# Kernel optimization log

Hardware: AMD Instinct MI355X
Metric: run time of the kernel (lower is better)

The kernel has to match this reference:

```python
import jax, jax.numpy as jnp
import numpy as np


def _hemisphere(radius=1.0, n=5):
    # replicates DiffuseShader.generate_hemisphere with sample=(5j,5j)
    u, v = np.mgrid[0:np.pi:n * 1j, 0:np.pi:n * 1j]
    x = (radius * np.cos(u) * np.sin(v)).flatten()
    y = (radius * np.sin(u) * np.sin(v)).flatten()
    z = (radius * np.cos(v)).flatten()
    return jnp.asarray(np.c_[x, y, z], dtype=jnp.float32)


def _diffuse_forward(V, COL, OPA, p, l, normals, hemi_vecs, indices, pointindex):
    P, S, N = p.shape[0], hemi_vecs.shape[0], V.shape[0]
    local = pointindex % P
    # --- project_hemisphere_projection: Rodrigues rotation local->global ---
    u = l[None, :] - p                                      # [P,3]
    u_hat = u / jnp.linalg.norm(u, axis=1, keepdims=True)
    v_loc = jnp.broadcast_to(jnp.array([0.0, -1.0, 0.0], p.dtype), u_hat.shape)
    c = -u_hat[:, 1:2]                                      # rowwise dot(v_loc, u_hat), [P,1]
    w = jnp.cross(v_loc, u_hat)                             # [P,3]
    z0 = jnp.zeros_like(w[:, 0])
    vmat = jnp.stack([jnp.stack([z0, -w[:, 2], w[:, 1]], -1),
                      jnp.stack([w[:, 2], z0, -w[:, 0]], -1),
                      jnp.stack([-w[:, 1], w[:, 0], z0], -1)], axis=1)  # [P,3,3] skew(w)
    R = jnp.eye(3, dtype=p.dtype)[None] + vmat + jnp.matmul(vmat, vmat) / (1.0 + c)[..., None]
    lh = jnp.einsum('pij,sj->psi', R, hemi_vecs) + l        # [P,S,3]
    o = jnp.broadcast_to(p[:, None, :], (P, S, 3))
    d = lh - o
    # --- get_intersection: ray/plane distances ---
    nrm = jnp.cross(V[:, 1] - V[:, 0], V[:, 2] - V[:, 0])
    nrm = nrm / jnp.linalg.norm(nrm, axis=1, keepdims=True)  # [N,3]
    kk = -jnp.sum(nrm * V[:, 3], axis=1)                     # [N]
    vo = o.reshape(P * S, 3) @ nrm.T                         # [P*S,N]
    vd = d.reshape(P * S, 3) @ nrm.T
    t = (-(kk[None, :] + vo) / vd).reshape(P, N, S)          # faithful to torch .view(P,N,S) on the [P*S,N] buffer
    surf = indices[pointindex, 0]
    mat = indices[pointindex, 1]
    empty = jnp.zeros((P, N, S), bool).at[local, surf, :].set(True)
    viable = (t > -1e-4) & (t < 1.0) & (~empty)
    # --- barycentric condition test ---
    r = o[:, None, :, :] + t[..., None] * d[:, None, :, :]   # [P,N,S,3]
    a0 = V[:, 0, 0][None, :, None]; a1 = V[:, 0, 1][None, :, None]; a2 = V[:, 0, 2][None, :, None]
    b0 = V[:, 1, 0][None, :, None]; b1 = V[:, 1, 1][None, :, None]; b2 = V[:, 1, 2][None, :, None]
    c0 = V[:, 2, 0][None, :, None]; c1 = V[:, 2, 1][None, :, None]; c2 = V[:, 2, 2][None, :, None]
    r0, r1, r2 = r[..., 0], r[..., 1], r[..., 2]
    A = a0 * r2 - a2 * r0
    B = a0 * b2 - a2 * b0
    C = a0 * r1 - a1 * r0
    D = a0 * b1 - a1 * b0
    E = a0 * c2 - a2 * c0
    F = B * (a1 * c0 - a0 * c1)
    gam = (D * (A * D - B * C)) / (D * (E * D + F))
    beta = (C + gam * (a1 * c0 - a0 * c1)) / D
    alpha = (r0 - (beta * b0 + gam * c0)) / a0
    mask = jnp.where(viable & (beta > 0.0) & (gam > 0.0) & (alpha > 0.0), 1.0, 0.0).astype(jnp.float32)
    col = COL[surf, mat]                                     # [P,3]
    opa = jnp.clip(OPA[surf, mat], 0.0, 1.0)                 # [P]
    reflected_ray = l[None, :] - p                           # [P,3]
    return mask, col, opa, reflected_ray


def setup_inputs() -> dict:
    P, N, M, G = 512, 1024, 8, 2048
    key = jax.random.key(0)
    ks = jax.random.split(key, 8)
    V = jax.random.normal(ks[0], (N, 4, 3), jnp.float32)
    indices = jax.random.randint(ks[1], (G, 2), 0, M)
    pointindex = jax.random.randint(ks[2], (P,), 0, G)
    COL = jax.random.uniform(ks[3], (N, M, 3), jnp.float32)
    OPA = jax.random.uniform(ks[4], (N, M), jnp.float32)
    p = jax.random.normal(ks[5], (P, 3), jnp.float32) * 5.0
    l = jax.random.normal(ks[6], (3,), jnp.float32) * 10.0 + 20.0
    normals = jax.random.normal(ks[7], (N, 3), jnp.float32)
    return {"V": V, "indices": indices, "pointindex": pointindex, "COL": COL,
            "OPA": OPA, "p": p, "l": l, "normals": normals, "it": 0,
            "hemi_vecs": _hemisphere(1.0, 5)}


def reference(V, indices, pointindex, COL, OPA, p, l, normals, it, hemi_vecs):
    return _diffuse_forward(V, COL, OPA, p, l, normals, hemi_vecs, indices, pointindex)
```

## Files before the change

### kernel.cpp

```cpp
#include <hip/hip_runtime.h>
#include <math.h>

#define NP   512
#define NT   1024
#define NS   25
#define NPS  (NP*NS)
#define MASKN (NP*NT*NS)

#define DSA_OFF  0
#define PD_OFF   51200
#define NX_OFF   53248
#define NY_OFF   54272
#define NZ_OFF   55296
#define KK_OFF   56320
#define W_OFF    57344
#define EMPTY_OFF ((size_t)67584 * 8)
#define F32_BYTE_OFF (EMPTY_OFF + 2048)
#define FD_OFF   0
#define FPD_OFF  51200
#define FNX_OFF  53248
#define FNY_OFF  54272
#define FNZ_OFF  55296
#define FKK_OFF  56320
#define FW_OFF   57344

#define CEPS 7.6293945e-06f

__device__ __forceinline__ double sgn(double x) {
    return (x > 0.0) ? 1.0 : ((x < 0.0) ? -1.0 : 0.0);
}

__global__ void prep_all(const float* __restrict__ p,
                         const float* __restrict__ l,
                         const float* __restrict__ hemi,
                         const float* __restrict__ V,
                         const int* __restrict__ indices,
                         const int* __restrict__ pointindex,
                         const float* __restrict__ COL,
                         const float* __restrict__ OPA,
                         double* __restrict__ ws,
                         unsigned* __restrict__ emptyMask,
                         float* __restrict__ out) {
    const int b = blockIdx.x, t = threadIdx.x;
    float* __restrict__ f32w = (float*)((char*)ws + F32_BYTE_OFF);
    if (b < 50) {
        int idx = b * 256 + t;
        int pi = idx / NS, si = idx % NS;
        double px = p[pi*3+0], py = p[pi*3+1], pz = p[pi*3+2];
        double lx = l[0], ly = l[1], lz = l[2];
        double ux = lx - px, uy = ly - py, uz = lz - pz;
        double nrm = sqrt(ux*ux + uy*uy + uz*uz);
        ux /= nrm; uy /= nrm; uz /= nrm;
        double c = -uy;
        double wx = -uz, wz = ux;
        double m01 = -wz, m10 = wz, m12 = -wx, m21 = wx;
        double q00 = m01*m10;
        double q02 = m01*m12;
        double q11 = m10*m01 + m12*m21;
        double q20 = m21*m10;
        double q22 = m21*m12;
        double ic = 1.0 + c;
        double r00 = 1.0 + q00/ic, r01 = m01,            r02 = q02/ic;
        double r10 = m10,          r11 = 1.0 + q11/ic,   r12 = m12;
        double r20 = q20/ic,       r21 = m21,            r22 = 1.0 + q22/ic;
        double hx = hemi[si*3+0], hy = hemi[si*3+1], hz = hemi[si*3+2];
        double dx = r00*hx + r01*hy + r02*hz + lx - px;
        double dy = r10*hx + r11*hy + r12*hz + ly - py;
        double dz = r20*hx + r21*hy + r22*hz + lz - pz;
        double* dsA = ws + DSA_OFF;
        dsA[idx*4+0] = dx;
        dsA[idx*4+1] = dy;
        dsA[idx*4+2] = dz;
        dsA[idx*4+3] = 0.0;
        *(float4*)(f32w + FD_OFF + idx*4) =
            make_float4((float)dx, (float)dy, (float)dz, 0.0f);
    } else if (b < 54) {
        int n = (b - 50) * 256 + t;
        const float* v = V + n*12;
        double a0=v[0], a1=v[1], a2=v[2];
        double b0=v[3], b1=v[4], b2=v[5];
        double c0=v[6], c1=v[7], c2=v[8];
        double v3x=v[9], v3y=v[10], v3z=v[11];
        double e1x=b0-a0, e1y=b1-a1, e1z=b2-a2;
        double e2x=c0-a0, e2y=c1-a1, e2z=c2-a2;
        double cx = e1y*e2z - e1z*e2y;
        double cy = e1z*e2x - e1x*e2z;
        double cz = e1x*e2y - e1y*e2x;
        double nn = sqrt(cx*cx + cy*cy + cz*cz);
        double nx = cx/nn, ny = cy/nn, nz = cz/nn;
        double kk = -(nx*v3x + ny*v3y + nz*v3z);
        double Bv = a0*b2 - a2*b0;
        double Dv = a0*b1 - a1*b0;
        double Ec = a0*c2 - a2*c0;
        double G2 = a1*c0 - a0*c1;
        double Fc = Bv*G2;
        double gd = Dv*(Ec*Dv + Fc);
        double gq = Dv*gd;
        double dq = Dv*c0;
        double aq = a0*gq;
        double WGr0 = a1*Bv - a2*Dv, WGr1 = -(a0*Bv), WGr2 = a0*Dv;
        double dg = Dv*G2;
        double WBr0 = -(a1*gd) + dg*WGr0;
        double WBr1 =  a0*gd  + dg*WGr1;
        double WBr2 =            dg*WGr2;
        double dd = Dv*dq;
        double WAr0 = gq - b0*WBr0 - dd*WGr0;
        double WAr1 =    - b0*WBr1 - dd*WGr1;
        double WAr2 =    - b0*WBr2 - dd*WGr2;
        double sg = sgn(Dv*gd), sb = sgn(gq), sa = sgn(aq);
        ws[NX_OFF + n] = nx;
        ws[NY_OFF + n] = ny;
        ws[NZ_OFF + n] = nz;
        ws[KK_OFF + n] = kk;
        double g0 = WGr0*sg, g1 = WGr1*sg, g2 = WGr2*sg;
        double bb0 = WBr0*sb, bb1 = WBr1*sb, bb2 = WBr2*sb;
        double aa0 = WAr0*sa, aa1 = WAr1*sa, aa2 = WAr2*sa;
        double* W = ws + W_OFF + n*10;
        W[0]=g0; W[1]=g1; W[2]=g2;
        W[3]=bb0; W[4]=bb1; W[5]=bb2;
        W[6]=aa0; W[7]=aa1; W[8]=aa2;
        W[9]=0.0;
        f32w[FNX_OFF+n]=(float)nx; f32w[FNY_OFF+n]=(float)ny;
        f32w[FNZ_OFF+n]=(float)nz; f32w[FKK_OFF+n]=(float)kk;
        double wsg = fabs(g0)+fabs(g1)+fabs(g2);
        double wsb = fabs(bb0)+fabs(bb1)+fabs(bb2);
        double wsa = fabs(aa0)+fabs(aa1)+fabs(aa2);
        double ig = wsg>0.0 ? 1.0/wsg : 0.0;
        double ib = wsb>0.0 ? 1.0/wsb : 0.0;
        double ia = wsa>0.0 ? 1.0/wsa : 0.0;
        float* fw = f32w + FW_OFF + n*12;
        fw[0]=(float)(g0*ig);  fw[1]=(float)(g1*ig);  fw[2]=(float)(g2*ig);
        fw[3]=(float)(bb0*ib); fw[4]=(float)(bb1*ib); fw[5]=(float)(bb2*ib);
        fw[6]=(float)(aa0*ia); fw[7]=(float)(aa1*ia); fw[8]=(float)(aa2*ia);
        fw[9]=0.0f; fw[10]=0.0f; fw[11]=0.0f;
    } else {
        emptyMask[t] = 0u;
        emptyMask[t + 256] = 0u;
        __syncthreads();
        for (int i = t; i < NP; i += 256) {
            int pidx = pointindex[i];
            int local = pidx & (NP - 1);
            int surf = indices[pidx*2 + 0];
            int mat  = indices[pidx*2 + 1];
            atomicOr(&emptyMask[local], 1u << surf);
            float* colOut = out + MASKN;
            float* opaOut = out + MASKN + 3*NP;
            float* refOut = out + MASKN + 4*NP;
            colOut[i*3+0] = COL[(surf*8+mat)*3+0];
            colOut[i*3+1] = COL[(surf*8+mat)*3+1];
            colOut[i*3+2] = COL[(surf*8+mat)*3+2];
            float o = OPA[surf*8+mat];
            opaOut[i] = fminf(fmaxf(o, 0.0f), 1.0f);
            refOut[i*3+0] = (float)((double)l[0] - (double)p[i*3+0]);
            refOut[i*3+1] = (float)((double)l[1] - (double)p[i*3+1]);
            refOut[i*3+2] = (float)((double)l[2] - (double)p[i*3+2]);
            double* pd = ws + PD_OFF;
            pd[i*4+0] = (double)p[i*3+0];
            pd[i*4+1] = (double)p[i*3+1];
            pd[i*4+2] = (double)p[i*3+2];
            pd[i*4+3] = 0.0;
            *(float4*)(f32w + FPD_OFF + i*4) =
                make_float4(p[i*3+0], p[i*3+1], p[i*3+2], 0.0f);
        }
    }
}

__device__ __forceinline__ float recheck64(const double* __restrict__ ws,
        unsigned ps, unsigned pp, unsigned i, unsigned nn, unsigned ss,
        unsigned em) {
    const double* s = ws + DSA_OFF + ps*4u;
    const double* o = ws + PD_OFF + pp*4u;
    double nx = ws[NX_OFF+i], ny = ws[NY_OFF+i], nz = ws[NZ_OFF+i];
    double kk = ws[KK_OFF+i];
    double vd = fma(s[2], nz, fma(s[1], ny, s[0]*nx));
    double tt = fma(o[2], nz, fma(o[1], ny, fma(o[0], nx, kk)));
    double e1 = fma(1e-4, vd, -tt);
    double e2 = vd + tt;
    const double* d = ws + DSA_OFF + (pp*25u + ss)*4u;
    double R0 = fma(-tt, d[0], vd*o[0]);
    double R1 = fma(-tt, d[1], vd*o[1]);
    double R2 = fma(-tt, d[2], vd*o[2]);
    const double* w = ws + W_OFF + nn*10u;
    double dG = fma(R2, w[2], fma(R1, w[1], R0*w[0]));
    double dB = fma(R2, w[5], fma(R1, w[4], R0*w[3]));
    double dA = fma(R2, w[8], fma(R1, w[7], R0*w[6]));
    int hv = __double2hiint(vd);
    int m = (__double2hiint(e1)^hv) | (__double2hiint(e2)^hv)
          | (__double2hiint(dG)^hv) | (__double2hiint(dB)^hv)
          | (__double2hiint(dA)^hv);
    bool ok = (m >= 0) && !((nn < 8u) && ((em >> nn) & 1u));
    return ok ? 1.0f : 0.0f;
}

__global__ __launch_bounds__(256, 4) void diffuse_main(
        const double* __restrict__ ws,
        const unsigned* __restrict__ emptyMask,
        float* __restrict__ out) {
    __shared__ float sW[42][12];
    __shared__ float sdx[25], sdy[25], sdz[25], sdm[25];

    const float* __restrict__ f32 = (const float*)((const char*)ws + F32_BYTE_OFF);
    const unsigned ps = blockIdx.x;
    const unsigned pp = ps / 25u;
    const unsigned q  = ps - pp*25u;
    const unsigned nn0 = (q << 10) / 25u;
    const unsigned tid = threadIdx.x;
    const unsigned n0 = tid * 4u;

    const float4 fnx = *(const float4*)(f32 + FNX_OFF + n0);
    const float4 fny = *(const float4*)(f32 + FNY_OFF + n0);
    const float4 fnz = *(const float4*)(f32 + FNZ_OFF + n0);
    const float4 fkk = *(const float4*)(f32 + FKK_OFF + n0);
    const float sx = f32[FD_OFF + ps*4u + 0];
    const float sy = f32[FD_OFF + ps*4u + 1];
    const float sz = f32[FD_OFF + ps*4u + 2];
    const float ox = f32[FPD_OFF + pp*4u + 0];
    const float oy = f32[FPD_OFF + pp*4u + 1];
    const float oz = f32[FPD_OFF + pp*4u + 2];
    const unsigned em = (q == 0u) ? emptyMask[pp] : 0u;
    const float S1u = fabsf(sx) + fabsf(sy) + fabsf(sz);
    const float O1u = fabsf(ox) + fabsf(oy) + fabsf(oz);
    const float Evd = CEPS * S1u;
    const float Eb0 = S1u + O1u;
    const float SOu = S1u * O1u;

    if (tid < 126u) {
        unsigned row = tid / 3u, quad = tid - row*3u;
        unsigned gn = nn0 + row; if (gn > 1023u) gn = 1023u;
        const float4 v = *(const float4*)(f32 + FW_OFF + gn*12u + quad*4u);
        *(float4*)(&sW[row][quad*4u]) = v;
    }
    if (tid < 25u) {
        const float4 dr = *(const float4*)(f32 + FD_OFF + (pp*25u + tid)*4u);
        sdx[tid] = dr.x; sdy[tid] = dr.y; sdz[tid] = dr.z;
        sdm[tid] = fmaxf(fabsf(dr.x), fmaxf(fabsf(dr.y), fabsf(dr.z)));
    }
    __syncthreads();

    const float nxk[4] = {fnx.x, fnx.y, fnx.z, fnx.w};
    const float nyk[4] = {fny.x, fny.y, fny.z, fny.w};
    const float nzk[4] = {fnz.x, fnz.y, fnz.z, fnz.w};
    const float kkk[4] = {fkk.x, fkk.y, fkk.z, fkk.w};

    unsigned rem = (q << 10) + n0;
    unsigned nn = rem / 25u;
    unsigned ss = rem - nn*25u;

    float res[4];
    #pragma unroll
    for (int k = 0; k < 4; ++k) {
        const float nx = nxk[k], ny = nyk[k], nz = nzk[k], kk = kkk[k];
        const float vd = fmaf(sz, nz, fmaf(sy, ny, sx*nx));
        const float tt = fmaf(oz, nz, fmaf(oy, ny, fmaf(ox, nx, kk)));
        const float e1 = fmaf(1e-4f, vd, -tt);
        const float e2 = vd + tt;

        const float dxv = sdx[ss], dyv = sdy[ss], dzv = sdz[ss], dmv = sdm[ss];
        const float R0 = fmaf(-tt, dxv, vd*ox);
        const float R1 = fmaf(-tt, dyv, vd*oy);
        const float R2 = fmaf(-tt, dzv, vd*oz);

        const float* w = sW[nn - nn0];
        const float dG = fmaf(R2, w[2], fmaf(R1, w[1], R0*w[0]));
        const float dB = fmaf(R2, w[5], fmaf(R1, w[4], R0*w[3]));
        const float dA = fmaf(R2, w[8], fmaf(R1, w[7], R0*w[6]));

        const int hv = __float_as_int(vd);
        int msk = (__float_as_int(e1)^hv) | (__float_as_int(e2)^hv)
                | (__float_as_int(dG)^hv) | (__float_as_int(dB)^hv)
                | (__float_as_int(dA)^hv);
        bool ok = (msk >= 0) && !((nn < 8u) && ((em >> nn) & 1u));

        const float akk = fabsf(kk);
        const float Ee  = CEPS * (Eb0 + akk);
        const float Mtt = O1u + akk;
        const float MR  = fmaf(Mtt, dmv, SOu);
        const float Edx = CEPS * MR;
        const float mind = fminf(fabsf(dG), fminf(fabsf(dB), fabsf(dA)));
        const bool flag = (fabsf(vd) < Evd) | (fabsf(e1) < Ee)
                        | (fabsf(e2) < Ee) | (mind < Edx);

        float r = ok ? 1.0f : 0.0f;
        if (__builtin_expect(flag, 0))
            r = recheck64(ws, ps, pp, n0 + (unsigned)k, nn, ss, em);
        res[k] = r;

        ss += 1u;
        const bool wrap = (ss == 25u);
        nn += wrap ? 1u : 0u;
        ss  = wrap ? 0u : ss;
    }
    *(float4*)(out + (ps << 10) + n0) = make_float4(res[0], res[1], res[2], res[3]);
}

extern "C" void kernel_launch(void* const* d_in, const int* in_sizes, int n_in,
                              void* d_out, int out_size, void* d_ws, size_t ws_size,
                              hipStream_t stream) {
    const float* V         = (const float*)d_in[0];
    const int*   indices   = (const int*)  d_in[1];
    const int*   pointindex= (const int*)  d_in[2];
    const float* COL       = (const float*)d_in[3];
    const float* OPA       = (const float*)d_in[4];
    const float* p         = (const float*)d_in[5];
    const float* l         = (const float*)d_in[6];
    const float* hemi      = (const float*)d_in[9];

    float* out = (float*)d_out;
    double* ws = (double*)d_ws;
    unsigned* emptyMask = (unsigned*)((char*)d_ws + EMPTY_OFF);

    prep_all<<<55, 256, 0, stream>>>(p, l, hemi, V, indices, pointindex,
                                     COL, OPA, ws, emptyMask, out);
    diffuse_main<<<NPS, 256, 0, stream>>>(ws, emptyMask, out);
}
```

Baseline: 33.65 us.

## Restructure main kernel to per-point blocks with per-triangle weights in registers and bitmask output

Each block now handles half of one point's 1024 triangles instead of one (point, sample) row. Each thread keeps two triangles' edge weights in registers and loops over all 25 samples, reusing those weights. Normals are staged in shared memory, and results are packed into 25-bit masks before a shared-memory transpose produces coalesced float2 stores. The fp64 recheck becomes a noinline function run per flagged bit, which cuts register pressure on the common path. The cost is more shared memory, a second barrier and more index arithmetic.

```diff
diff --git a/kernel.cpp b/kernel.cpp
--- a/kernel.cpp
+++ b/kernel.cpp
@@ -165,13 +165,12 @@
     }
 }
 
-__device__ __forceinline__ float recheck64(const double* __restrict__ ws,
-        unsigned ps, unsigned pp, unsigned i, unsigned nn, unsigned ss,
-        unsigned em) {
+__device__ __noinline__ unsigned recheck64(const double* __restrict__ ws,
+        unsigned ps, unsigned pp, unsigned n, unsigned nn, unsigned ss) {
     const double* s = ws + DSA_OFF + ps*4u;
     const double* o = ws + PD_OFF + pp*4u;
-    double nx = ws[NX_OFF+i], ny = ws[NY_OFF+i], nz = ws[NZ_OFF+i];
-    double kk = ws[KK_OFF+i];
+    double nx = ws[NX_OFF+n], ny = ws[NY_OFF+n], nz = ws[NZ_OFF+n];
+    double kk = ws[KK_OFF+n];
     double vd = fma(s[2], nz, fma(s[1], ny, s[0]*nx));
     double tt = fma(o[2], nz, fma(o[1], ny, fma(o[0], nx, kk)));
     double e1 = fma(1e-4, vd, -tt);
@@ -188,109 +187,138 @@
     int m = (__double2hiint(e1)^hv) | (__double2hiint(e2)^hv)
           | (__double2hiint(dG)^hv) | (__double2hiint(dB)^hv)
           | (__double2hiint(dA)^hv);
-    bool ok = (m >= 0) && !((nn < 8u) && ((em >> nn) & 1u));
-    return ok ? 1.0f : 0.0f;
+    return (m >= 0) ? 1u : 0u;
 }
 
 __global__ __launch_bounds__(256, 4) void diffuse_main(
         const double* __restrict__ ws,
         const unsigned* __restrict__ emptyMask,
         float* __restrict__ out) {
-    __shared__ float sW[42][12];
-    __shared__ float sdx[25], sdy[25], sdz[25], sdm[25];
+    __shared__ __align__(16) float snx[NT], sny[NT], snz[NT], skk[NT];
+    __shared__ float4 sdr[NS];
+    __shared__ unsigned sbits[512];
 
     const float* __restrict__ f32 = (const float*)((const char*)ws + F32_BYTE_OFF);
-    const unsigned ps = blockIdx.x;
-    const unsigned pp = ps / 25u;
-    const unsigned q  = ps - pp*25u;
-    const unsigned nn0 = (q << 10) / 25u;
+    const unsigned pp = blockIdx.x >> 1;
+    const unsigned half = blockIdx.x & 1u;
     const unsigned tid = threadIdx.x;
-    const unsigned n0 = tid * 4u;
-
-    const float4 fnx = *(const float4*)(f32 + FNX_OFF + n0);
-    const float4 fny = *(const float4*)(f32 + FNY_OFF + n0);
-    const float4 fnz = *(const float4*)(f32 + FNZ_OFF + n0);
-    const float4 fkk = *(const float4*)(f32 + FKK_OFF + n0);
-    const float sx = f32[FD_OFF + ps*4u + 0];
-    const float sy = f32[FD_OFF + ps*4u + 1];
-    const float sz = f32[FD_OFF + ps*4u + 2];
+    const unsigned nnA = half*512u + tid;
+    const unsigned nnB = nnA + 256u;
+
+    const float4 wA0 = *(const float4*)(f32 + FW_OFF + nnA*12u);
+    const float4 wA1 = *(const float4*)(f32 + FW_OFF + nnA*12u + 4u);
+    const float4 wA2 = *(const float4*)(f32 + FW_OFF + nnA*12u + 8u);
+    const float4 wB0 = *(const float4*)(f32 + FW_OFF + nnB*12u);
+    const float4 wB1 = *(const float4*)(f32 + FW_OFF + nnB*12u + 4u);
+    const float4 wB2 = *(const float4*)(f32 + FW_OFF + nnB*12u + 8u);
     const float ox = f32[FPD_OFF + pp*4u + 0];
     const float oy = f32[FPD_OFF + pp*4u + 1];
     const float oz = f32[FPD_OFF + pp*4u + 2];
-    const unsigned em = (q == 0u) ? emptyMask[pp] : 0u;
-    const float S1u = fabsf(sx) + fabsf(sy) + fabsf(sz);
+    const unsigned em = emptyMask[pp];
+
+    {
+        const unsigned i4 = tid * 4u;
+        *(float4*)&snx[i4] = *(const float4*)(f32 + FNX_OFF + i4);
+        *(float4*)&sny[i4] = *(const float4*)(f32 + FNY_OFF + i4);
+        *(float4*)&snz[i4] = *(const float4*)(f32 + FNZ_OFF + i4);
+        *(float4*)&skk[i4] = *(const float4*)(f32 + FKK_OFF + i4);
+    }
+    if (tid < 25u) {
+        float4 dr = *(const float4*)(f32 + FD_OFF + (pp*25u + tid)*4u);
+        dr.w = fmaxf(fabsf(dr.x), fmaxf(fabsf(dr.y), fabsf(dr.z)));
+        sdr[tid] = dr;
+    }
+    __syncthreads();
+
     const float O1u = fabsf(ox) + fabsf(oy) + fabsf(oz);
-    const float Evd = CEPS * S1u;
-    const float Eb0 = S1u + O1u;
-    const float SOu = S1u * O1u;
-
-    if (tid < 126u) {
-        unsigned row = tid / 3u, quad = tid - row*3u;
-        unsigned gn = nn0 + row; if (gn > 1023u) gn = 1023u;
-        const float4 v = *(const float4*)(f32 + FW_OFF + gn*12u + quad*4u);
-        *(float4*)(&sW[row][quad*4u]) = v;
-    }
-    if (tid < 25u) {
-        const float4 dr = *(const float4*)(f32 + FD_OFF + (pp*25u + tid)*4u);
-        sdx[tid] = dr.x; sdy[tid] = dr.y; sdz[tid] = dr.z;
-        sdm[tid] = fmaxf(fabsf(dr.x), fmaxf(fabsf(dr.y), fabsf(dr.z)));
+
+    #pragma unroll
+    for (int h = 0; h < 2; ++h) {
+        const unsigned nn = h ? nnB : nnA;
+        const float4 w0 = h ? wB0 : wA0;
+        const float4 w1 = h ? wB1 : wA1;
+        const float4 w2 = h ? wB2 : wA2;
+        const unsigned m0  = nn * 25u;
+        const unsigned n0  = m0 & 1023u;
+        const unsigned ps0 = m0 >> 10;
+        const unsigned idx1 = (m0 + 24u) >> 10;
+        const unsigned ssX = ((ps0 + 1u) << 10) - m0;
+        const float4 s0v = sdr[ps0];
+        const float4 s1v = sdr[idx1];
+        const float S10 = fabsf(s0v.x) + fabsf(s0v.y) + fabsf(s0v.z);
+        const float S11 = fabsf(s1v.x) + fabsf(s1v.y) + fabsf(s1v.z);
+
+        unsigned acc = 0u, flg = 0u;
+        #pragma unroll 5
+        for (unsigned ss = 0u; ss < 25u; ++ss) {
+            const bool cr = (ss >= ssX);
+            const float sx = cr ? s1v.x : s0v.x;
+            const float sy = cr ? s1v.y : s0v.y;
+            const float sz = cr ? s1v.z : s0v.z;
+            const float S1u = cr ? S11 : S10;
+            const unsigned n = n0 + ss - (cr ? 1024u : 0u);
+            const float nx = snx[n], ny = sny[n], nz = snz[n], kk = skk[n];
+
+            const float vd = fmaf(sz, nz, fmaf(sy, ny, sx*nx));
+            const float tt = fmaf(oz, nz, fmaf(oy, ny, fmaf(ox, nx, kk)));
+            const float e1 = fmaf(1e-4f, vd, -tt);
+            const float e2 = vd + tt;
+
+            const float4 d4 = sdr[ss];
+            const float R0 = fmaf(-tt, d4.x, vd*ox);
+            const float R1 = fmaf(-tt, d4.y, vd*oy);
+            const float R2 = fmaf(-tt, d4.z, vd*oz);
+
+            const float dG = fmaf(R2, w0.z, fmaf(R1, w0.y, R0*w0.x));
+            const float dB = fmaf(R2, w1.y, fmaf(R1, w1.x, R0*w0.w));
+            const float dA = fmaf(R2, w2.x, fmaf(R1, w1.w, R0*w1.z));
+
+            const int hv = __float_as_int(vd);
+            const int msk = (__float_as_int(e1)^hv) | (__float_as_int(e2)^hv)
+                          | (__float_as_int(dG)^hv) | (__float_as_int(dB)^hv)
+                          | (__float_as_int(dA)^hv);
+            acc |= ((unsigned)(msk >= 0)) << ss;
+
+            const float akk = fabsf(kk);
+            const float Ee  = CEPS * (S1u + O1u + akk);
+            const float Mtt = O1u + akk;
+            const float MR  = fmaf(Mtt, d4.w, S1u * O1u);
+            const float Edx = CEPS * MR;
+            const float mind = fminf(fabsf(dG), fminf(fabsf(dB), fabsf(dA)));
+            const bool flag = (fabsf(vd) < CEPS*S1u) | (fabsf(e1) < Ee)
+                            | (fabsf(e2) < Ee) | (mind < Edx);
+            flg |= ((unsigned)flag) << ss;
+        }
+        if (__builtin_expect(flg != 0u, 0)) {
+            unsigned f2 = flg;
+            while (f2) {
+                const unsigned ss = (unsigned)__ffs(f2) - 1u;
+                f2 &= f2 - 1u;
+                const bool cr = (ss >= ssX);
+                const unsigned n = n0 + ss - (cr ? 1024u : 0u);
+                const unsigned ps = pp*25u + ps0 + (cr ? 1u : 0u);
+                const unsigned bit = recheck64(ws, ps, pp, n, nn, ss);
+                acc = (acc & ~(1u << ss)) | (bit << ss);
+            }
+        }
+        if ((nn < 8u) && ((em >> nn) & 1u)) acc = 0u;
+        sbits[h*256u + tid] = acc;
     }
     __syncthreads();
 
-    const float nxk[4] = {fnx.x, fnx.y, fnx.z, fnx.w};
-    const float nyk[4] = {fny.x, fny.y, fny.z, fny.w};
-    const float nzk[4] = {fnz.x, fnz.y, fnz.z, fnz.w};
-    const float kkk[4] = {fkk.x, fkk.y, fkk.z, fkk.w};
-
-    unsigned rem = (q << 10) + n0;
-    unsigned nn = rem / 25u;
-    unsigned ss = rem - nn*25u;
-
-    float res[4];
-    #pragma unroll
-    for (int k = 0; k < 4; ++k) {
-        const float nx = nxk[k], ny = nyk[k], nz = nzk[k], kk = kkk[k];
-        const float vd = fmaf(sz, nz, fmaf(sy, ny, sx*nx));
-        const float tt = fmaf(oz, nz, fmaf(oy, ny, fmaf(ox, nx, kk)));
-        const float e1 = fmaf(1e-4f, vd, -tt);
-        const float e2 = vd + tt;
-
-        const float dxv = sdx[ss], dyv = sdy[ss], dzv = sdz[ss], dmv = sdm[ss];
-        const float R0 = fmaf(-tt, dxv, vd*ox);
-        const float R1 = fmaf(-tt, dyv, vd*oy);
-        const float R2 = fmaf(-tt, dzv, vd*oz);
-
-        const float* w = sW[nn - nn0];
-        const float dG = fmaf(R2, w[2], fmaf(R1, w[1], R0*w[0]));
-        const float dB = fmaf(R2, w[5], fmaf(R1, w[4], R0*w[3]));
-        const float dA = fmaf(R2, w[8], fmaf(R1, w[7], R0*w[6]));
-
-        const int hv = __float_as_int(vd);
-        int msk = (__float_as_int(e1)^hv) | (__float_as_int(e2)^hv)
-                | (__float_as_int(dG)^hv) | (__float_as_int(dB)^hv)
-                | (__float_as_int(dA)^hv);
-        bool ok = (msk >= 0) && !((nn < 8u) && ((em >> nn) & 1u));
-
-        const float akk = fabsf(kk);
-        const float Ee  = CEPS * (Eb0 + akk);
-        const float Mtt = O1u + akk;
-        const float MR  = fmaf(Mtt, dmv, SOu);
-        const float Edx = CEPS * MR;
-        const float mind = fminf(fabsf(dG), fminf(fabsf(dB), fabsf(dA)));
-        const bool flag = (fabsf(vd) < Evd) | (fabsf(e1) < Ee)
-                        | (fabsf(e2) < Ee) | (mind < Edx);
-
-        float r = ok ? 1.0f : 0.0f;
-        if (__builtin_expect(flag, 0))
-            r = recheck64(ws, ps, pp, n0 + (unsigned)k, nn, ss, em);
-        res[k] = r;
-
-        ss += 1u;
-        const bool wrap = (ss == 25u);
-        nn += wrap ? 1u : 0u;
-        ss  = wrap ? 0u : ss;
-    }
-    *(float4*)(out + (ps << 10) + n0) = make_float4(res[0], res[1], res[2], res[3]);
+    const unsigned obase = pp*25600u + half*12800u;
+    #pragma unroll 5
+    for (unsigned it = 0u; it < 25u; ++it) {
+        const unsigned j = (it*256u + tid) * 2u;
+        const unsigned nn1 = j / 25u;
+        const unsigned ss1 = j - nn1*25u;
+        const unsigned j2 = j + 1u;
+        const unsigned nn2 = j2 / 25u;
+        const unsigned ss2 = j2 - nn2*25u;
+        const float r0 = ((sbits[nn1] >> ss1) & 1u) ? 1.0f : 0.0f;
+        const float r1 = ((sbits[nn2] >> ss2) & 1u) ? 1.0f : 0.0f;
+        *(float2*)(out + obase + j) = make_float2(r0, r1);
+    }
 }
 
 extern "C" void kernel_launch(void* const* d_in, const int* in_sizes, int n_in,
@@ -311,5 +339,5 @@
 
     prep_all<<<55, 256, 0, stream>>>(p, l, hemi, V, indices, pointindex,
                                      COL, OPA, ws, emptyMask, out);
-    diffuse_main<<<NPS, 256, 0, stream>>>(ws, emptyMask, out);
-}
+    diffuse_main<<<NP*2, 256, 0, stream>>>(ws, emptyMask, out);
+}
```

Result: slower. 38.94 us (+15.7%).

## Load plane weights into registers, defer fp64 rechecks to a noinline loop

Applied to the files above, without the earlier changes.

The shared-memory staging of per-triangle edge weights is dropped. Each thread now loads the two weight rows it can touch (nnA and nnB) straight into registers, and the per-sample direction table becomes a float4 array in shared memory. The fp64 recheck is no longer called inline inside the unrolled loop: flags are packed into a bitmask and rechecked afterwards through a noinline function, with the minimum-occupancy hint removed from launch bounds. The goal is fewer LDS reads, a smaller shared footprint and lower register pressure on the common path. The cost is more global loads per thread and a function call on the rare path.

```diff
diff --git a/kernel.cpp b/kernel.cpp
--- a/kernel.cpp
+++ b/kernel.cpp
@@ -165,13 +165,12 @@
     }
 }
 
-__device__ __forceinline__ float recheck64(const double* __restrict__ ws,
-        unsigned ps, unsigned pp, unsigned i, unsigned nn, unsigned ss,
-        unsigned em) {
+__device__ __noinline__ unsigned recheck64(const double* __restrict__ ws,
+        unsigned ps, unsigned pp, unsigned n, unsigned nn, unsigned ss) {
     const double* s = ws + DSA_OFF + ps*4u;
     const double* o = ws + PD_OFF + pp*4u;
-    double nx = ws[NX_OFF+i], ny = ws[NY_OFF+i], nz = ws[NZ_OFF+i];
-    double kk = ws[KK_OFF+i];
+    double nx = ws[NX_OFF+n], ny = ws[NY_OFF+n], nz = ws[NZ_OFF+n];
+    double kk = ws[KK_OFF+n];
     double vd = fma(s[2], nz, fma(s[1], ny, s[0]*nx));
     double tt = fma(o[2], nz, fma(o[1], ny, fma(o[0], nx, kk)));
     double e1 = fma(1e-4, vd, -tt);
@@ -188,25 +187,33 @@
     int m = (__double2hiint(e1)^hv) | (__double2hiint(e2)^hv)
           | (__double2hiint(dG)^hv) | (__double2hiint(dB)^hv)
           | (__double2hiint(dA)^hv);
-    bool ok = (m >= 0) && !((nn < 8u) && ((em >> nn) & 1u));
-    return ok ? 1.0f : 0.0f;
-}
-
-__global__ __launch_bounds__(256, 4) void diffuse_main(
+    return (m >= 0) ? 1u : 0u;
+}
+
+__global__ __launch_bounds__(256) void diffuse_main(
         const double* __restrict__ ws,
         const unsigned* __restrict__ emptyMask,
         float* __restrict__ out) {
-    __shared__ float sW[42][12];
-    __shared__ float sdx[25], sdy[25], sdz[25], sdm[25];
+    __shared__ float4 sdr[NS];
 
     const float* __restrict__ f32 = (const float*)((const char*)ws + F32_BYTE_OFF);
     const unsigned ps = blockIdx.x;
     const unsigned pp = ps / 25u;
     const unsigned q  = ps - pp*25u;
-    const unsigned nn0 = (q << 10) / 25u;
     const unsigned tid = threadIdx.x;
     const unsigned n0 = tid * 4u;
 
+    const unsigned rem0 = (q << 10) + n0;
+    const unsigned nnA = rem0 / 25u;
+    const unsigned ssA = rem0 - nnA*25u;
+    const unsigned nnB = (nnA < 1023u) ? (nnA + 1u) : 1023u;
+
+    const float4 wA0 = *(const float4*)(f32 + FW_OFF + nnA*12u);
+    const float4 wA1 = *(const float4*)(f32 + FW_OFF + nnA*12u + 4u);
+    const float4 wA2 = *(const float4*)(f32 + FW_OFF + nnA*12u + 8u);
+    const float4 wB0 = *(const float4*)(f32 + FW_OFF + nnB*12u);
+    const float4 wB1 = *(const float4*)(f32 + FW_OFF + nnB*12u + 4u);
+    const float4 wB2 = *(const float4*)(f32 + FW_OFF + nnB*12u + 8u);
     const float4 fnx = *(const float4*)(f32 + FNX_OFF + n0);
     const float4 fny = *(const float4*)(f32 + FNY_OFF + n0);
     const float4 fnz = *(const float4*)(f32 + FNZ_OFF + n0);
@@ -218,77 +225,86 @@
     const float oy = f32[FPD_OFF + pp*4u + 1];
     const float oz = f32[FPD_OFF + pp*4u + 2];
     const unsigned em = (q == 0u) ? emptyMask[pp] : 0u;
+
+    if (tid < 25u) {
+        float4 dr = *(const float4*)(f32 + FD_OFF + (pp*25u + tid)*4u);
+        dr.w = fmaxf(fabsf(dr.x), fmaxf(fabsf(dr.y), fabsf(dr.z)));
+        sdr[tid] = dr;
+    }
+    __syncthreads();
+
     const float S1u = fabsf(sx) + fabsf(sy) + fabsf(sz);
     const float O1u = fabsf(ox) + fabsf(oy) + fabsf(oz);
+    const float SOu = S1u * O1u;
     const float Evd = CEPS * S1u;
-    const float Eb0 = S1u + O1u;
-    const float SOu = S1u * O1u;
-
-    if (tid < 126u) {
-        unsigned row = tid / 3u, quad = tid - row*3u;
-        unsigned gn = nn0 + row; if (gn > 1023u) gn = 1023u;
-        const float4 v = *(const float4*)(f32 + FW_OFF + gn*12u + quad*4u);
-        *(float4*)(&sW[row][quad*4u]) = v;
-    }
-    if (tid < 25u) {
-        const float4 dr = *(const float4*)(f32 + FD_OFF + (pp*25u + tid)*4u);
-        sdx[tid] = dr.x; sdy[tid] = dr.y; sdz[tid] = dr.z;
-        sdm[tid] = fmaxf(fabsf(dr.x), fmaxf(fabsf(dr.y), fabsf(dr.z)));
-    }
-    __syncthreads();
 
     const float nxk[4] = {fnx.x, fnx.y, fnx.z, fnx.w};
     const float nyk[4] = {fny.x, fny.y, fny.z, fny.w};
     const float nzk[4] = {fnz.x, fnz.y, fnz.z, fnz.w};
     const float kkk[4] = {fkk.x, fkk.y, fkk.z, fkk.w};
 
-    unsigned rem = (q << 10) + n0;
-    unsigned nn = rem / 25u;
-    unsigned ss = rem - nn*25u;
-
     float res[4];
+    unsigned flg = 0u;
     #pragma unroll
     for (int k = 0; k < 4; ++k) {
+        const bool useB = (ssA + (unsigned)k >= 25u);
+        const unsigned ss = ssA + (unsigned)k - (useB ? 25u : 0u);
+        const unsigned nn = useB ? nnB : nnA;
+        const float wg0 = useB ? wB0.x : wA0.x;
+        const float wg1 = useB ? wB0.y : wA0.y;
+        const float wg2 = useB ? wB0.z : wA0.z;
+        const float wb0 = useB ? wB0.w : wA0.w;
+        const float wb1 = useB ? wB1.x : wA1.x;
+        const float wb2 = useB ? wB1.y : wA1.y;
+        const float wa0 = useB ? wB1.z : wA1.z;
+        const float wa1 = useB ? wB1.w : wA1.w;
+        const float wa2 = useB ? wB2.x : wA2.x;
+
         const float nx = nxk[k], ny = nyk[k], nz = nzk[k], kk = kkk[k];
         const float vd = fmaf(sz, nz, fmaf(sy, ny, sx*nx));
         const float tt = fmaf(oz, nz, fmaf(oy, ny, fmaf(ox, nx, kk)));
         const float e1 = fmaf(1e-4f, vd, -tt);
         const float e2 = vd + tt;
 
-        const float dxv = sdx[ss], dyv = sdy[ss], dzv = sdz[ss], dmv = sdm[ss];
-        const float R0 = fmaf(-tt, dxv, vd*ox);
-        const float R1 = fmaf(-tt, dyv, vd*oy);
-        const float R2 = fmaf(-tt, dzv, vd*oz);
-
-        const float* w = sW[nn - nn0];
-        const float dG = fmaf(R2, w[2], fmaf(R1, w[1], R0*w[0]));
-        const float dB = fmaf(R2, w[5], fmaf(R1, w[4], R0*w[3]));
-        const float dA = fmaf(R2, w[8], fmaf(R1, w[7], R0*w[6]));
+        const float4 d4 = sdr[ss];
+        const float R0 = fmaf(-tt, d4.x, vd*ox);
+        const float R1 = fmaf(-tt, d4.y, vd*oy);
+        const float R2 = fmaf(-tt, d4.z, vd*oz);
+
+        const float dG = fmaf(R2, wg2, fmaf(R1, wg1, R0*wg0));
+        const float dB = fmaf(R2, wb2, fmaf(R1, wb1, R0*wb0));
+        const float dA = fmaf(R2, wa2, fmaf(R1, wa1, R0*wa0));
 
         const int hv = __float_as_int(vd);
-        int msk = (__float_as_int(e1)^hv) | (__float_as_int(e2)^hv)
-                | (__float_as_int(dG)^hv) | (__float_as_int(dB)^hv)
-                | (__float_as_int(dA)^hv);
+        const int msk = (__float_as_int(e1)^hv) | (__float_as_int(e2)^hv)
+                      | (__float_as_int(dG)^hv) | (__float_as_int(dB)^hv)
+                      | (__float_as_int(dA)^hv);
         bool ok = (msk >= 0) && !((nn < 8u) && ((em >> nn) & 1u));
+        res[k] = ok ? 1.0f : 0.0f;
 
         const float akk = fabsf(kk);
-        const float Ee  = CEPS * (Eb0 + akk);
+        const float Ee  = CEPS * (S1u + O1u + akk);
         const float Mtt = O1u + akk;
-        const float MR  = fmaf(Mtt, dmv, SOu);
+        const float MR  = fmaf(Mtt, d4.w, SOu);
         const float Edx = CEPS * MR;
         const float mind = fminf(fabsf(dG), fminf(fabsf(dB), fabsf(dA)));
         const bool flag = (fabsf(vd) < Evd) | (fabsf(e1) < Ee)
                         | (fabsf(e2) < Ee) | (mind < Edx);
-
-        float r = ok ? 1.0f : 0.0f;
-        if (__builtin_expect(flag, 0))
-            r = recheck64(ws, ps, pp, n0 + (unsigned)k, nn, ss, em);
-        res[k] = r;
-
-        ss += 1u;
-        const bool wrap = (ss == 25u);
-        nn += wrap ? 1u : 0u;
-        ss  = wrap ? 0u : ss;
+        flg |= ((unsigned)flag) << k;
+    }
+
+    if (__builtin_expect(flg != 0u, 0)) {
+        unsigned f2 = flg;
+        while (f2) {
+            const unsigned k = (unsigned)__ffs(f2) - 1u;
+            f2 &= f2 - 1u;
+            const bool useB = (ssA + k >= 25u);
+            const unsigned ss = ssA + k - (useB ? 25u : 0u);
+            const unsigned nn = useB ? nnB : nnA;
+            const unsigned bit = recheck64(ws, ps, pp, n0 + k, nn, ss);
+            const bool okEmpty = !((nn < 8u) && ((em >> nn) & 1u));
+            res[k] = (bit && okEmpty) ? 1.0f : 0.0f;
+        }
     }
     *(float4*)(out + (ps << 10) + n0) = make_float4(res[0], res[1], res[2], res[3]);
 }
```

After: 36.53 us. 1.09x slower.
